# Kernel tuning notes

Measured on AMD Instinct MI355X. Metric: run time of the kernel, lower is better.

Reference implementation:

```python
import jax, jax.numpy as jnp
import numpy as np

EMBD = 384
FFN = 4 * EMBD
T = 200
NH = 6
HS = EMBD // NH
B = 256


def _layernorm(x, g, b, eps=1e-5):
    m = jnp.mean(x, axis=-1, keepdims=True)
    v = jnp.mean((x - m) ** 2, axis=-1, keepdims=True)
    return (x - m) * jax.lax.rsqrt(v + eps) * g + b


def setup_inputs() -> dict:
    key = jax.random.key(0)
    ks = jax.random.split(key, 10)
    s = EMBD ** -0.5
    return {
        "x": jax.random.normal(ks[0], (B, T, EMBD), dtype=jnp.float32),
        "Wq": jax.random.normal(ks[1], (EMBD, EMBD), dtype=jnp.float32) * s,
        "Wk": jax.random.normal(ks[2], (EMBD, EMBD), dtype=jnp.float32) * s,
        "Wv": jax.random.normal(ks[3], (EMBD, EMBD), dtype=jnp.float32) * s,
        "Wproj": jax.random.normal(ks[4], (EMBD, EMBD), dtype=jnp.float32) * s,
        "bproj": jnp.zeros((EMBD,), dtype=jnp.float32),
        "W1": jax.random.normal(ks[5], (EMBD, FFN), dtype=jnp.float32) * s,
        "b1": jnp.zeros((FFN,), dtype=jnp.float32),
        "W2": jax.random.normal(ks[6], (FFN, EMBD), dtype=jnp.float32) * (FFN ** -0.5),
        "b2": jnp.zeros((EMBD,), dtype=jnp.float32),
        "g1": jnp.ones((EMBD,), dtype=jnp.float32),
        "be1": jnp.zeros((EMBD,), dtype=jnp.float32),
        "g2": jnp.ones((EMBD,), dtype=jnp.float32),
        "be2": jnp.zeros((EMBD,), dtype=jnp.float32),
    }


def reference(x, Wq, Wk, Wv, Wproj, bproj, W1, b1, W2, b2, g1, be1, g2, be2):
    # pre-LN attention
    h = _layernorm(x, g1, be1)
    Bb, Tt, _ = h.shape
    q = (h @ Wq).reshape(Bb, Tt, NH, HS)
    k = (h @ Wk).reshape(Bb, Tt, NH, HS)
    v = (h @ Wv).reshape(Bb, Tt, NH, HS)
    # NOTE: original scales by C**-0.5 where C = embd (not head_size)
    scores = jnp.einsum("bthd,bshd->bhts", q, k) * (EMBD ** -0.5)
    causal = jnp.tril(jnp.ones((Tt, Tt), dtype=bool))
    scores = jnp.where(causal, scores, -jnp.inf)
    wei = jax.nn.softmax(scores, axis=-1)
    att = jnp.einsum("bhts,bshd->bthd", wei, v).reshape(Bb, Tt, EMBD)
    x = x + att @ Wproj + bproj
    # FFN (dropout is identity in eval mode)
    h2 = _layernorm(x, g2, be2)
    ffn = jax.nn.relu(h2 @ W1 + b1) @ W2 + b2
    return x + ffn
```

## Files before the change

### kernel.cpp

```cpp
#include <hip/hip_runtime.h>

#define EMBD 384
#define FFN_DIM 1536
#define T_SEQ 200
#define NHEAD 6
#define BATCH 256

typedef __bf16 bf16x8_t __attribute__((ext_vector_type(8)));
typedef short s16x8_t __attribute__((ext_vector_type(8)));
typedef float f32x4_t __attribute__((ext_vector_type(4)));

__device__ __forceinline__ float bf2f(unsigned short h) {
  return __builtin_bit_cast(float, (unsigned)h << 16);
}
__device__ __forceinline__ unsigned short f2bf(float f) {
  unsigned u = __builtin_bit_cast(unsigned, f);
  u += 0x7fffu + ((u >> 16) & 1u);
  return (unsigned short)(u >> 16);
}
__device__ __forceinline__ void async_cp16(const void* g, void* l) {
  __builtin_amdgcn_global_load_lds(
      (const __attribute__((address_space(1))) unsigned int*)g,
      (__attribute__((address_space(3))) unsigned int*)l, 16, 0, 0);
}

__global__ void detect_dtype(const unsigned short* __restrict__ xr, int* __restrict__ flag) {
  int tid = threadIdx.x;
  int cnt = 0;
  for (int i = tid; i < 4096; i += 256) {
    float a = fabsf(bf2f(xr[2 * i]));
    cnt += (a > 1e-5f && a < 32.f) ? 1 : 0;
  }
#pragma unroll
  for (int off = 32; off; off >>= 1) cnt += __shfl_xor(cnt, off);
  __shared__ int tot;
  if (tid == 0) tot = 0;
  __syncthreads();
  if ((tid & 63) == 0) atomicAdd(&tot, cnt);
  __syncthreads();
  if (tid == 0) *flag = (tot > 2048) ? 1 : 0;
}

__global__ void cvt_all(const void* bproj, const void* b1, const void* b2,
                        const void* g1, const void* be1, const void* g2, const void* be2,
                        float* __restrict__ dst, const int* __restrict__ flagp) {
  int i = blockIdx.x * 256 + threadIdx.x;
  if (i >= 3840) return;
  const void* src; int loc;
  if (i < 384)       { src = bproj; loc = i; }
  else if (i < 1920) { src = b1;    loc = i - 384; }
  else if (i < 2304) { src = b2;    loc = i - 1920; }
  else if (i < 2688) { src = g1;    loc = i - 2304; }
  else if (i < 3072) { src = be1;   loc = i - 2688; }
  else if (i < 3456) { src = g2;    loc = i - 3072; }
  else               { src = be2;   loc = i - 3456; }
  dst[i] = (*flagp) ? bf2f(((const unsigned short*)src)[loc]) : ((const float*)src)[loc];
}

static constexpr size_t OFF_WQKV  = 0;
static constexpr size_t OFF_WPROJ = OFF_WQKV  + (size_t)1152 * 384 * 2;
static constexpr size_t OFF_W1    = OFF_WPROJ + (size_t)384 * 384 * 2;
static constexpr size_t OFF_W2    = OFF_W1    + (size_t)1536 * 384 * 2;
static constexpr size_t OFF_BIAS  = OFF_W2    + (size_t)384 * 1536 * 2;
static constexpr size_t OFF_FLAG  = OFF_BIAS  + 4096 * 4;
static constexpr size_t OFF_DYN   = OFF_FLAG + 256;

__global__ void pack_all(const void* Wq, const void* Wk, const void* Wv, const void* Wp,
                         const void* W1, const void* W2, char* __restrict__ ws,
                         const int* __restrict__ flagp) {
  int idx = blockIdx.x * 256 + threadIdx.x;
  if (idx >= 1769472) return;
  const void* W; unsigned short* Wt; int loc, K, N, ldt;
  if (idx < 589824) {
    int which = idx / 147456;
    loc = idx - which * 147456; K = 384; N = 384; ldt = 384;
    if (which == 0)      { W = Wq; Wt = (unsigned short*)(ws + OFF_WQKV); }
    else if (which == 1) { W = Wk; Wt = (unsigned short*)(ws + OFF_WQKV) + 147456; }
    else if (which == 2) { W = Wv; Wt = (unsigned short*)(ws + OFF_WQKV) + 294912; }
    else                 { W = Wp; Wt = (unsigned short*)(ws + OFF_WPROJ); }
  } else if (idx < 1179648) {
    loc = idx - 589824; K = 384; N = 1536; ldt = 384;
    W = W1; Wt = (unsigned short*)(ws + OFF_W1);
  } else {
    loc = idx - 1179648; K = 1536; N = 384; ldt = 1536;
    W = W2; Wt = (unsigned short*)(ws + OFF_W2);
  }
  int k = loc / N, n = loc % N;
  unsigned short v = (*flagp) ? ((const unsigned short*)W)[loc]
                              : f2bf(((const float*)W)[loc]);
  Wt[(size_t)n * ldt + k] = v;
}

__global__ __launch_bounds__(256) void ln_kernel(const void* __restrict__ xin, int row0,
                                                 const float* __restrict__ g,
                                                 const float* __restrict__ be,
                                                 unsigned short* __restrict__ out,
                                                 int isbf_mode, const int* __restrict__ flagp) {
  int rloc = blockIdx.x * 4 + (threadIdx.x >> 6);
  int lane = threadIdx.x & 63;
  int isbf = (isbf_mode >= 0) ? isbf_mode : *flagp;
  size_t row = (size_t)(row0 + rloc);
  float v[8];
  float sum = 0.f;
  const int act = lane < 48;
  const int c0 = lane * 8;
  if (act) {
    if (isbf) {
      s16x8_t xv = *(const s16x8_t*)((const unsigned short*)xin + row * EMBD + c0);
#pragma unroll
      for (int i = 0; i < 8; ++i) { v[i] = bf2f((unsigned short)xv[i]); sum += v[i]; }
    } else {
      const float* xr = (const float*)xin + row * EMBD + c0;
#pragma unroll
      for (int i = 0; i < 8; ++i) { v[i] = xr[i]; sum += v[i]; }
    }
  } else {
#pragma unroll
    for (int i = 0; i < 8; ++i) v[i] = 0.f;
  }
#pragma unroll
  for (int off = 32; off; off >>= 1) sum += __shfl_xor(sum, off);
  float mean = sum * (1.f / EMBD);
  float var = 0.f;
  if (act) {
#pragma unroll
    for (int i = 0; i < 8; ++i) { float d = v[i] - mean; var += d * d; }
  }
#pragma unroll
  for (int off = 32; off; off >>= 1) var += __shfl_xor(var, off);
  float rstd = rsqrtf(var * (1.f / EMBD) + 1e-5f);
  if (act) {
    s16x8_t ov;
#pragma unroll
    for (int i = 0; i < 8; ++i)
      ov[i] = (short)f2bf((v[i] - mean) * rstd * g[c0 + i] + be[c0 + i]);
    *(s16x8_t*)(out + (size_t)rloc * EMBD + c0) = ov;
  }
}

template <int MODE>
__global__ __launch_bounds__(256, 3) void gemm_kernel(
    const unsigned short* __restrict__ A, int lda,
    const unsigned short* __restrict__ Bt, int K,
    const float* __restrict__ bias,
    const void* __restrict__ R, int ldr, int rrow0,
    void* __restrict__ Cv, int ldc, int crow0,
    int Mrows, int NX, int NY, const int* __restrict__ flagp) {
  __shared__ unsigned short As[128 * 64];
  __shared__ unsigned short Bs[128 * 64];
  const int g = blockIdx.x;
  const int xcd = g & 7, s = g >> 3;
  const int j = s / NX, xn = s - j * NX;
  const int y = xcd + 8 * j;
  if (y >= NY) return;
  const int n0 = xn * 128;
  const int m0 = y * 128;
  const int tid = threadIdx.x;
  const int wv = tid >> 6, lane = tid & 63;
  const int wr = wv >> 1, wc = wv & 1;
  const int l = lane & 15, quad = lane >> 4;
  f32x4_t acc[4][4];
#pragma unroll
  for (int i = 0; i < 4; ++i)
#pragma unroll
    for (int jj = 0; jj < 4; ++jj) acc[i][jj] = (f32x4_t){0.f, 0.f, 0.f, 0.f};

  for (int kc = 0; kc < K; kc += 64) {
#pragma unroll
    for (int i = 0; i < 4; ++i) {
      int c = (wv * 4 + i) * 64 + lane;
      int row = c >> 3;
      int kk = ((c & 7) ^ (row & 7)) * 8;
      int ar = m0 + row;
      if (ar >= Mrows) ar = Mrows - 1;
      async_cp16(A + (size_t)ar * lda + kc + kk, As + (wv * 4 + i) * 512);
    }
#pragma unroll
    for (int i = 0; i < 4; ++i) {
      int c = (wv * 4 + i) * 64 + lane;
      int row = c >> 3;
      int kk = ((c & 7) ^ (row & 7)) * 8;
      async_cp16(Bt + (size_t)(n0 + row) * K + kc + kk, Bs + (wv * 4 + i) * 512);
    }
    __syncthreads();
#pragma unroll
    for (int ks = 0; ks < 2; ++ks) {
      bf16x8_t af[4], bfr[4];
#pragma unroll
      for (int gg = 0; gg < 4; ++gg) {
        int row = wr * 64 + gg * 16 + l;
        int ch = row * 8 + ((quad + ks * 4) ^ (row & 7));
        af[gg] = *(const bf16x8_t*)&As[ch * 8];
        int nrw = wc * 64 + gg * 16 + l;
        int nch = nrw * 8 + ((quad + ks * 4) ^ (nrw & 7));
        bfr[gg] = *(const bf16x8_t*)&Bs[nch * 8];
      }
#pragma unroll
      for (int i = 0; i < 4; ++i)
#pragma unroll
        for (int jj = 0; jj < 4; ++jj)
          acc[i][jj] = __builtin_amdgcn_mfma_f32_16x16x32_bf16(af[i], bfr[jj], acc[i][jj], 0, 0, 0);
    }
    __syncthreads();
  }

  int isbf = flagp ? *flagp : 1;
#pragma unroll
  for (int i = 0; i < 4; ++i) {
#pragma unroll
    for (int jj = 0; jj < 4; ++jj) {
#pragma unroll
      for (int r = 0; r < 4; ++r) {
        int row = m0 + wr * 64 + i * 16 + quad * 4 + r;
        int col = n0 + wc * 64 + jj * 16 + l;
        if (row >= Mrows) continue;
        float v = acc[i][jj][r];
        if (MODE == 0) {
          ((unsigned short*)Cv)[(size_t)row * ldc + col] = f2bf(v);
        } else if (MODE == 1) {
          v += bias[col];
          ((unsigned short*)Cv)[(size_t)row * ldc + col] = f2bf(fmaxf(v, 0.f));
        } else if (MODE == 2) {
          size_t ridx = (size_t)(rrow0 + row) * ldr + col;
          float rv = isbf ? bf2f(((const unsigned short*)R)[ridx]) : ((const float*)R)[ridx];
          ((unsigned short*)Cv)[(size_t)row * ldc + col] = f2bf(v + bias[col] + rv);
        } else {
          float rv = bf2f(((const unsigned short*)R)[(size_t)row * ldr + col]);
          float o = v + bias[col] + rv;
          size_t cidx = (size_t)(crow0 + row) * ldc + col;
          if (isbf)
            ((unsigned short*)Cv)[cidx] = f2bf(o);
          else
            ((float*)Cv)[cidx] = o;
        }
      }
    }
  }
}

__global__ __launch_bounds__(256, 2) void attn_kernel(const unsigned short* __restrict__ qkv,
                                                      unsigned short* __restrict__ att) {
  __shared__ unsigned short Vt[64 * 232];
  __shared__ unsigned short Ps[64 * 232];
  const int bh = blockIdx.x;
  const int b = bh / NHEAD, h = bh % NHEAD;
  const size_t base = (size_t)b * T_SEQ * 1152;
  const int tid = threadIdx.x;
  const int w = tid >> 6, lane = tid & 63;
  const int l = lane & 15, quad = lane >> 4;

  for (int idx = tid; idx < 1600; idx += 256) {
    int s = idx >> 3, d0 = (idx & 7) * 8;
    s16x8_t vv = *(const s16x8_t*)(qkv + base + (size_t)s * 1152 + 768 + h * 64 + d0);
#pragma unroll
    for (int i = 0; i < 8; ++i) Vt[(d0 + i) * 232 + s] = (unsigned short)vv[i];
  }
  for (int idx = tid; idx < 64 * 32; idx += 256) {
    int d = idx >> 5, c = idx & 31;
    Vt[d * 232 + 200 + c] = 0;
  }
  {
    s16x8_t zz = {0, 0, 0, 0, 0, 0, 0, 0};
    for (int idx = tid; idx < 1856; idx += 256) *(s16x8_t*)&Ps[idx * 8] = zz;
  }
  __syncthreads();

  const float scale = 0.051031036307982884f;
  const unsigned short* kp = qkv + base + 384 + h * 64;
  for (int t0 = 0; t0 < T_SEQ; t0 += 64) {
    if (t0 + w * 16 >= T_SEQ) continue;
    int tq = t0 + w * 16 + l;
    const unsigned short* qp = qkv + base + (size_t)tq * 1152 + h * 64;
    bf16x8_t qa0 = *(const bf16x8_t*)(qp + quad * 8);
    bf16x8_t qa1 = *(const bf16x8_t*)(qp + 32 + quad * 8);
    const int cmax = (t0 >> 4) + w + 1;
    f32x4_t sa[13];
#pragma unroll
    for (int c = 0; c < 13; ++c) {
      if (c < cmax) {
        const unsigned short* kr = kp + (size_t)(c * 16 + l) * 1152;
        bf16x8_t kb0 = *(const bf16x8_t*)(kr + quad * 8);
        bf16x8_t kb1 = *(const bf16x8_t*)(kr + 32 + quad * 8);
        f32x4_t z = (f32x4_t){0.f, 0.f, 0.f, 0.f};
        z = __builtin_amdgcn_mfma_f32_16x16x32_bf16(qa0, kb0, z, 0, 0, 0);
        sa[c] = __builtin_amdgcn_mfma_f32_16x16x32_bf16(qa1, kb1, z, 0, 0, 0);
      }
    }
#pragma unroll
    for (int r = 0; r < 4; ++r) {
      int t = t0 + w * 16 + quad * 4 + r;
      float tv[13];
      float mx = -1e30f;
#pragma unroll
      for (int c = 0; c < 13; ++c) {
        if (c < cmax) {
          int col = c * 16 + l;
          float v = sa[c][r] * scale;
          tv[c] = (col <= t) ? v : -1e30f;
          mx = fmaxf(mx, tv[c]);
        }
      }
#pragma unroll
      for (int off = 1; off < 16; off <<= 1) mx = fmaxf(mx, __shfl_xor(mx, off));
      float sum = 0.f;
#pragma unroll
      for (int c = 0; c < 13; ++c) {
        if (c < cmax) {
          float p = __expf(tv[c] - mx);
          tv[c] = p;
          sum += p;
        }
      }
#pragma unroll
      for (int off = 1; off < 16; off <<= 1) sum += __shfl_xor(sum, off);
      float inv = 1.f / sum;
#pragma unroll
      for (int c = 0; c < 13; ++c) {
        if (c < cmax)
          Ps[(w * 16 + quad * 4 + r) * 232 + c * 16 + l] = f2bf(tv[c] * inv);
      }
    }
    int smax = t0 + w * 16 + 16;
    if (smax > T_SEQ) smax = T_SEQ;
    const int ksteps = (smax + 31) >> 5;
    f32x4_t oa[4];
#pragma unroll
    for (int d = 0; d < 4; ++d) oa[d] = (f32x4_t){0.f, 0.f, 0.f, 0.f};
    for (int ks = 0; ks < ksteps; ++ks) {
      bf16x8_t pa = *(const bf16x8_t*)&Ps[(w * 16 + l) * 232 + ks * 32 + quad * 8];
#pragma unroll
      for (int d = 0; d < 4; ++d) {
        bf16x8_t vb = *(const bf16x8_t*)&Vt[(d * 16 + l) * 232 + ks * 32 + quad * 8];
        oa[d] = __builtin_amdgcn_mfma_f32_16x16x32_bf16(pa, vb, oa[d], 0, 0, 0);
      }
    }
#pragma unroll
    for (int d = 0; d < 4; ++d) {
#pragma unroll
      for (int r = 0; r < 4; ++r) {
        int t = t0 + w * 16 + quad * 4 + r;
        if (t < T_SEQ)
          att[((size_t)b * T_SEQ + t) * EMBD + h * 64 + d * 16 + l] = f2bf(oa[d][r]);
      }
    }
  }
}

extern "C" void kernel_launch(void* const* d_in, const int* in_sizes, int n_in,
                              void* d_out, int out_size, void* d_ws, size_t ws_size,
                              hipStream_t stream) {
  const void* x     = d_in[0];
  const void* Wq    = d_in[1];
  const void* Wk    = d_in[2];
  const void* Wv    = d_in[3];
  const void* Wproj = d_in[4];
  const void* bproj = d_in[5];
  const void* W1    = d_in[6];
  const void* b1    = d_in[7];
  const void* W2    = d_in[8];
  const void* b2    = d_in[9];
  const void* g1    = d_in[10];
  const void* be1   = d_in[11];
  const void* g2    = d_in[12];
  const void* be2   = d_in[13];

  char* ws = (char*)d_ws;
  unsigned short* wqkv_t  = (unsigned short*)(ws + OFF_WQKV);
  unsigned short* wproj_t = (unsigned short*)(ws + OFF_WPROJ);
  unsigned short* w1_t    = (unsigned short*)(ws + OFF_W1);
  unsigned short* w2_t    = (unsigned short*)(ws + OFF_W2);
  float*          bias_f  = (float*)(ws + OFF_BIAS);
  int*            flag    = (int*)(ws + OFF_FLAG);

  int Bc = BATCH;
  while (Bc > 1 && OFF_DYN + (size_t)Bc * T_SEQ * 6144 > ws_size) Bc >>= 1;
  if (OFF_DYN + (size_t)Bc * T_SEQ * 6144 > ws_size) return;
  const int NC = BATCH / Bc;
  const int Mc = Bc * T_SEQ;
  const int NY = (Mc + 127) / 128;
  const int NYpad = (NY + 7) & ~7;

  char* bufA = ws + OFF_DYN;
  char* bufB = bufA + (size_t)Mc * 2304;
  char* bufC = bufB + (size_t)Mc * 768;
  unsigned short* qkv = (unsigned short*)bufA;
  unsigned short* x2  = (unsigned short*)bufA;
  unsigned short* h2  = (unsigned short*)(bufA + (size_t)Mc * 768);
  unsigned short* hb  = (unsigned short*)bufB;
  unsigned short* mid = (unsigned short*)bufC;

  detect_dtype<<<1, 256, 0, stream>>>((const unsigned short*)x, flag);
  cvt_all<<<15, 256, 0, stream>>>(bproj, b1, b2, g1, be1, g2, be2, bias_f, flag);
  pack_all<<<6912, 256, 0, stream>>>(Wq, Wk, Wv, Wproj, W1, W2, ws, flag);

  for (int c = 0; c < NC; ++c) {
    const int row0 = c * Bc * T_SEQ;
    ln_kernel<<<Mc / 4, 256, 0, stream>>>(x, row0, bias_f + 2304, bias_f + 2688, hb, -1, flag);
    gemm_kernel<0><<<9 * NYpad, 256, 0, stream>>>(
        hb, 384, wqkv_t, 384, nullptr, nullptr, 0, 0, qkv, 1152, 0, Mc, 9, NY, nullptr);
    attn_kernel<<<Bc * NHEAD, 256, 0, stream>>>(qkv, hb);
    gemm_kernel<2><<<3 * NYpad, 256, 0, stream>>>(
        hb, 384, wproj_t, 384, bias_f + 0, x, 384, row0, x2, 384, 0, Mc, 3, NY, flag);
    ln_kernel<<<Mc / 4, 256, 0, stream>>>(x2, 0, bias_f + 3072, bias_f + 3456, h2, 1, nullptr);
    gemm_kernel<1><<<12 * NYpad, 256, 0, stream>>>(
        h2, 384, w1_t, 384, bias_f + 384, nullptr, 0, 0, mid, 1536, 0, Mc, 12, NY, nullptr);
    gemm_kernel<3><<<3 * NYpad, 256, 0, stream>>>(
        mid, 1536, w2_t, 1536, bias_f + 1920, x2, 384, 0, d_out, 384, row0, Mc, 3, NY, flag);
  }
}
```

Before: 679.3 us.

## Tile weight transpose via LDS, add wide-N FFN1 GEMM, shrink attention LDS

Result: slower. 792.8 us (+16.7%).

```diff
diff --git a/kernel.cpp b/kernel.cpp
--- a/kernel.cpp
+++ b/kernel.cpp
@@ -23,6 +23,14 @@
       (const __attribute__((address_space(1))) unsigned int*)g,
       (__attribute__((address_space(3))) unsigned int*)l, 16, 0, 0);
 }
+
+static constexpr size_t OFF_WQKV  = 0;
+static constexpr size_t OFF_WPROJ = OFF_WQKV  + (size_t)1152 * 384 * 2;
+static constexpr size_t OFF_W1    = OFF_WPROJ + (size_t)384 * 384 * 2;
+static constexpr size_t OFF_W2    = OFF_W1    + (size_t)1536 * 384 * 2;
+static constexpr size_t OFF_BIAS  = OFF_W2    + (size_t)384 * 1536 * 2;
+static constexpr size_t OFF_FLAG  = OFF_BIAS  + 4096 * 4;
+static constexpr size_t OFF_DYN   = OFF_FLAG + 256;
 
 __global__ void detect_dtype(const unsigned short* __restrict__ xr, int* __restrict__ flag) {
   int tid = threadIdx.x;
@@ -57,38 +65,47 @@
   dst[i] = (*flagp) ? bf2f(((const unsigned short*)src)[loc]) : ((const float*)src)[loc];
 }
 
-static constexpr size_t OFF_WQKV  = 0;
-static constexpr size_t OFF_WPROJ = OFF_WQKV  + (size_t)1152 * 384 * 2;
-static constexpr size_t OFF_W1    = OFF_WPROJ + (size_t)384 * 384 * 2;
-static constexpr size_t OFF_W2    = OFF_W1    + (size_t)1536 * 384 * 2;
-static constexpr size_t OFF_BIAS  = OFF_W2    + (size_t)384 * 1536 * 2;
-static constexpr size_t OFF_FLAG  = OFF_BIAS  + 4096 * 4;
-static constexpr size_t OFF_DYN   = OFF_FLAG + 256;
-
-__global__ void pack_all(const void* Wq, const void* Wk, const void* Wv, const void* Wp,
-                         const void* W1, const void* W2, char* __restrict__ ws,
-                         const int* __restrict__ flagp) {
-  int idx = blockIdx.x * 256 + threadIdx.x;
-  if (idx >= 1769472) return;
-  const void* W; unsigned short* Wt; int loc, K, N, ldt;
-  if (idx < 589824) {
-    int which = idx / 147456;
-    loc = idx - which * 147456; K = 384; N = 384; ldt = 384;
-    if (which == 0)      { W = Wq; Wt = (unsigned short*)(ws + OFF_WQKV); }
-    else if (which == 1) { W = Wk; Wt = (unsigned short*)(ws + OFF_WQKV) + 147456; }
-    else if (which == 2) { W = Wv; Wt = (unsigned short*)(ws + OFF_WQKV) + 294912; }
-    else                 { W = Wp; Wt = (unsigned short*)(ws + OFF_WPROJ); }
-  } else if (idx < 1179648) {
-    loc = idx - 589824; K = 384; N = 1536; ldt = 384;
-    W = W1; Wt = (unsigned short*)(ws + OFF_W1);
+__global__ __launch_bounds__(256) void pack_tr(const void* Wq, const void* Wk,
+                                               const void* Wv, const void* Wp,
+                                               const void* W1, const void* W2,
+                                               char* __restrict__ ws,
+                                               const int* __restrict__ flagp) {
+  __shared__ unsigned short T[64 * 80];
+  int t = blockIdx.x;
+  const void* W; unsigned short* Wt; int N, ldt, k0, n0;
+  if (t < 144) {
+    int which = t / 36, r = t % 36;
+    k0 = (r / 6) * 64; n0 = (r % 6) * 64; N = 384;
+    if (which < 3) { W = (which == 0 ? Wq : which == 1 ? Wk : Wv);
+                     Wt = (unsigned short*)(ws + OFF_WQKV) + which * 147456; ldt = 384; }
+    else           { W = Wp; Wt = (unsigned short*)(ws + OFF_WPROJ); ldt = 384; }
+  } else if (t < 288) {
+    int r = t - 144; k0 = (r / 24) * 64; n0 = (r % 24) * 64; N = 1536;
+    W = W1; Wt = (unsigned short*)(ws + OFF_W1); ldt = 384;
   } else {
-    loc = idx - 1179648; K = 1536; N = 384; ldt = 1536;
-    W = W2; Wt = (unsigned short*)(ws + OFF_W2);
-  }
-  int k = loc / N, n = loc % N;
-  unsigned short v = (*flagp) ? ((const unsigned short*)W)[loc]
-                              : f2bf(((const float*)W)[loc]);
-  Wt[(size_t)n * ldt + k] = v;
+    int r = t - 288; k0 = (r / 6) * 64; n0 = (r % 6) * 64; N = 384;
+    W = W2; Wt = (unsigned short*)(ws + OFF_W2); ldt = 1536;
+  }
+  const int tid = threadIdx.x;
+  const int rr = tid >> 2, cc = (tid & 3) * 16;
+  if (*flagp) {
+    const unsigned short* Ws = (const unsigned short*)W;
+    *(s16x8_t*)&T[rr * 80 + cc] = *(const s16x8_t*)&Ws[(size_t)(k0 + rr) * N + n0 + cc];
+    *(s16x8_t*)&T[rr * 80 + cc + 8] = *(const s16x8_t*)&Ws[(size_t)(k0 + rr) * N + n0 + cc + 8];
+    __syncthreads();
+    s16x8_t o0, o1;
+#pragma unroll
+    for (int j = 0; j < 8; ++j) o0[j] = (short)T[(cc + j) * 80 + rr];
+#pragma unroll
+    for (int j = 0; j < 8; ++j) o1[j] = (short)T[(cc + 8 + j) * 80 + rr];
+    *(s16x8_t*)&Wt[(size_t)(n0 + rr) * ldt + k0 + cc] = o0;
+    *(s16x8_t*)&Wt[(size_t)(n0 + rr) * ldt + k0 + cc + 8] = o1;
+  } else {
+    const float* Wf = (const float*)W;
+#pragma unroll
+    for (int j = 0; j < 16; ++j)
+      Wt[(size_t)(n0 + cc + j) * ldt + k0 + rr] = f2bf(Wf[(size_t)(k0 + rr) * N + n0 + cc + j]);
+  }
 }
 
 __global__ __launch_bounds__(256) void ln_kernel(const void* __restrict__ xin, int row0,
@@ -238,10 +255,93 @@
   }
 }
 
-__global__ __launch_bounds__(256, 2) void attn_kernel(const unsigned short* __restrict__ qkv,
+__global__ __launch_bounds__(256, 2) void gemm_wide(
+    const unsigned short* __restrict__ A, int lda,
+    const unsigned short* __restrict__ Bt, int K,
+    const float* __restrict__ bias,
+    void* __restrict__ Cv, int ldc,
+    int Mrows, int NX, int NY) {
+  __shared__ unsigned short As[128 * 64];
+  __shared__ unsigned short Bs[256 * 64];
+  const int g = blockIdx.x;
+  const int xcd = g & 7, s = g >> 3;
+  const int j = s / NX, xn = s - j * NX;
+  const int y = xcd + 8 * j;
+  if (y >= NY) return;
+  const int n0 = xn * 256;
+  const int m0 = y * 128;
+  const int tid = threadIdx.x;
+  const int wv = tid >> 6, lane = tid & 63;
+  const int wr = wv >> 1, wc = wv & 1;
+  const int l = lane & 15, quad = lane >> 4;
+  f32x4_t acc[4][8];
+#pragma unroll
+  for (int i = 0; i < 4; ++i)
+#pragma unroll
+    for (int jj = 0; jj < 8; ++jj) acc[i][jj] = (f32x4_t){0.f, 0.f, 0.f, 0.f};
+
+  for (int kc = 0; kc < K; kc += 64) {
+#pragma unroll
+    for (int i = 0; i < 4; ++i) {
+      int c = (wv * 4 + i) * 64 + lane;
+      int row = c >> 3;
+      int kk = ((c & 7) ^ (row & 7)) * 8;
+      int ar = m0 + row;
+      if (ar >= Mrows) ar = Mrows - 1;
+      async_cp16(A + (size_t)ar * lda + kc + kk, As + (wv * 4 + i) * 512);
+    }
+#pragma unroll
+    for (int i = 0; i < 8; ++i) {
+      int c = (wv * 8 + i) * 64 + lane;
+      int row = c >> 3;
+      int kk = ((c & 7) ^ (row & 7)) * 8;
+      async_cp16(Bt + (size_t)(n0 + row) * K + kc + kk, Bs + (wv * 8 + i) * 512);
+    }
+    __syncthreads();
+#pragma unroll
+    for (int ks = 0; ks < 2; ++ks) {
+      bf16x8_t af[4], bfr[8];
+#pragma unroll
+      for (int gg = 0; gg < 4; ++gg) {
+        int row = wr * 64 + gg * 16 + l;
+        int ch = row * 8 + ((quad + ks * 4) ^ (row & 7));
+        af[gg] = *(const bf16x8_t*)&As[ch * 8];
+      }
+#pragma unroll
+      for (int jj = 0; jj < 8; ++jj) {
+        int nrw = wc * 128 + jj * 16 + l;
+        int nch = nrw * 8 + ((quad + ks * 4) ^ (nrw & 7));
+        bfr[jj] = *(const bf16x8_t*)&Bs[nch * 8];
+      }
+#pragma unroll
+      for (int i = 0; i < 4; ++i)
+#pragma unroll
+        for (int jj = 0; jj < 8; ++jj)
+          acc[i][jj] = __builtin_amdgcn_mfma_f32_16x16x32_bf16(af[i], bfr[jj], acc[i][jj], 0, 0, 0);
+    }
+    __syncthreads();
+  }
+
+#pragma unroll
+  for (int i = 0; i < 4; ++i) {
+#pragma unroll
+    for (int jj = 0; jj < 8; ++jj) {
+#pragma unroll
+      for (int r = 0; r < 4; ++r) {
+        int row = m0 + wr * 64 + i * 16 + quad * 4 + r;
+        int col = n0 + wc * 128 + jj * 16 + l;
+        if (row >= Mrows) continue;
+        float v = acc[i][jj][r] + bias[col];
+        ((unsigned short*)Cv)[(size_t)row * ldc + col] = f2bf(fmaxf(v, 0.f));
+      }
+    }
+  }
+}
+
+__global__ __launch_bounds__(256, 3) void attn_kernel(const unsigned short* __restrict__ qkv,
                                                       unsigned short* __restrict__ att) {
-  __shared__ unsigned short Vt[64 * 232];
-  __shared__ unsigned short Ps[64 * 232];
+  __shared__ unsigned short Vt[64 * 208];
+  __shared__ unsigned short Ps[64 * 208];
   const int bh = blockIdx.x;
   const int b = bh / NHEAD, h = bh % NHEAD;
   const size_t base = (size_t)b * T_SEQ * 1152;
@@ -253,15 +353,15 @@
     int s = idx >> 3, d0 = (idx & 7) * 8;
     s16x8_t vv = *(const s16x8_t*)(qkv + base + (size_t)s * 1152 + 768 + h * 64 + d0);
 #pragma unroll
-    for (int i = 0; i < 8; ++i) Vt[(d0 + i) * 232 + s] = (unsigned short)vv[i];
-  }
-  for (int idx = tid; idx < 64 * 32; idx += 256) {
-    int d = idx >> 5, c = idx & 31;
-    Vt[d * 232 + 200 + c] = 0;
+    for (int i = 0; i < 8; ++i) Vt[(d0 + i) * 208 + s] = (unsigned short)vv[i];
+  }
+  for (int idx = tid; idx < 64 * 8; idx += 256) {
+    int d = idx >> 3, c = idx & 7;
+    Vt[d * 208 + 200 + c] = 0;
   }
   {
     s16x8_t zz = {0, 0, 0, 0, 0, 0, 0, 0};
-    for (int idx = tid; idx < 1856; idx += 256) *(s16x8_t*)&Ps[idx * 8] = zz;
+    for (int idx = tid; idx < 1664; idx += 256) *(s16x8_t*)&Ps[idx * 8] = zz;
   }
   __syncthreads();
 
@@ -317,21 +417,37 @@
 #pragma unroll
       for (int c = 0; c < 13; ++c) {
         if (c < cmax)
-          Ps[(w * 16 + quad * 4 + r) * 232 + c * 16 + l] = f2bf(tv[c] * inv);
-      }
-    }
-    int smax = t0 + w * 16 + 16;
-    if (smax > T_SEQ) smax = T_SEQ;
+          Ps[(w * 16 + quad * 4 + r) * 208 + c * 16 + l] = f2bf(tv[c] * inv);
+      }
+    }
+    int send = t0 + w * 16 + 16;
+    int smax = (send > 192) ? 192 : send;
     const int ksteps = (smax + 31) >> 5;
     f32x4_t oa[4];
 #pragma unroll
     for (int d = 0; d < 4; ++d) oa[d] = (f32x4_t){0.f, 0.f, 0.f, 0.f};
     for (int ks = 0; ks < ksteps; ++ks) {
-      bf16x8_t pa = *(const bf16x8_t*)&Ps[(w * 16 + l) * 232 + ks * 32 + quad * 8];
+      bf16x8_t pa = *(const bf16x8_t*)&Ps[(w * 16 + l) * 208 + ks * 32 + quad * 8];
 #pragma unroll
       for (int d = 0; d < 4; ++d) {
-        bf16x8_t vb = *(const bf16x8_t*)&Vt[(d * 16 + l) * 232 + ks * 32 + quad * 8];
+        bf16x8_t vb = *(const bf16x8_t*)&Vt[(d * 16 + l) * 208 + ks * 32 + quad * 8];
         oa[d] = __builtin_amdgcn_mfma_f32_16x16x32_bf16(pa, vb, oa[d], 0, 0, 0);
+      }
+    }
+    if (send > T_SEQ) {
+#pragma unroll
+      for (int r = 0; r < 4; ++r) {
+        int trow = w * 16 + quad * 4 + r;
+        float p[8];
+#pragma unroll
+        for (int ss = 0; ss < 8; ++ss) p[ss] = bf2f(Ps[trow * 208 + 192 + ss]);
+#pragma unroll
+        for (int d = 0; d < 4; ++d) {
+          float a = 0.f;
+#pragma unroll
+          for (int ss = 0; ss < 8; ++ss) a += p[ss] * bf2f(Vt[(d * 16 + l) * 208 + 192 + ss]);
+          oa[d][r] += a;
+        }
       }
     }
 #pragma unroll
@@ -391,7 +507,7 @@
 
   detect_dtype<<<1, 256, 0, stream>>>((const unsigned short*)x, flag);
   cvt_all<<<15, 256, 0, stream>>>(bproj, b1, b2, g1, be1, g2, be2, bias_f, flag);
-  pack_all<<<6912, 256, 0, stream>>>(Wq, Wk, Wv, Wproj, W1, W2, ws, flag);
+  pack_tr<<<432, 256, 0, stream>>>(Wq, Wk, Wv, Wproj, W1, W2, ws, flag);
 
   for (int c = 0; c < NC; ++c) {
     const int row0 = c * Bc * T_SEQ;
@@ -402,8 +518,8 @@
     gemm_kernel<2><<<3 * NYpad, 256, 0, stream>>>(
         hb, 384, wproj_t, 384, bias_f + 0, x, 384, row0, x2, 384, 0, Mc, 3, NY, flag);
     ln_kernel<<<Mc / 4, 256, 0, stream>>>(x2, 0, bias_f + 3072, bias_f + 3456, h2, 1, nullptr);
-    gemm_kernel<1><<<12 * NYpad, 256, 0, stream>>>(
-        h2, 384, w1_t, 384, bias_f + 384, nullptr, 0, 0, mid, 1536, 0, Mc, 12, NY, nullptr);
+    gemm_wide<<<6 * NYpad, 256, 0, stream>>>(
+        h2, 384, w1_t, 384, bias_f + 384, mid, 1536, Mc, 6, NY);
     gemm_kernel<3><<<3 * NYpad, 256, 0, stream>>>(
         mid, 1536, w2_t, 1536, bias_f + 1920, x2, 384, 0, d_out, 384, row0, Mc, 3, NY, flag);
   }
```
